# Performance work log

Measured on AMD Instinct MI355X. Metric: run time of the kernel, lower is better.

Reference implementation:

```python
import jax, jax.numpy as jnp
import numpy as np

PATCH = 3
ALPHA = 0.1


def _unfold3x3(x):
    # x: [B, C, H, W] -> [B, C*9, H, W], torch F.unfold with k=3, pad=1, stride=1
    B, C, H, W = x.shape
    p = PATCH // 2
    xp = jnp.pad(x, ((0, 0), (0, 0), (p, p), (p, p)))
    shifts = [xp[:, :, i:i + H, j:j + W] for i in range(PATCH) for j in range(PATCH)]
    # torch unfold orders (C, kh, kw); ordering is irrelevant for the dot-product
    # correlation, but we match it anyway: stack kernel positions after channel.
    out = jnp.stack(shifts, axis=2)  # [B, C, 9, H, W]
    return out.reshape(B, C * PATCH * PATCH, H, W)


def setup_inputs() -> dict:
    key = jax.random.key(0)
    k1, k2 = jax.random.split(key)
    x_lab = jax.random.normal(k1, (4, 3, 64, 64), dtype=jnp.float32)
    feature = jax.random.normal(k2, (4, 64, 64, 64), dtype=jnp.float32)
    return {"x_lab": x_lab, "feature": feature}


def reference(x_lab, feature):
    # scale_factor=1 and feature already at (H, W): both interpolates are identity.
    B, _, H, W = x_lab.shape
    N = H * W
    x_ab = x_lab.reshape(B, 3, N).transpose(0, 2, 1)          # [B, N, 3]
    lf = _unfold3x3(feature).reshape(B, -1, N)                 # [B, C*9, N]
    corr = jnp.einsum('bcn,bcm->bnm', lf, lf)                  # [B, N, N]
    attn = jax.nn.softmax(corr / ALPHA, axis=-1)
    weighted = jnp.einsum('bnm,bmc->bnc', attn, x_ab)          # [B, N, 3]
    return weighted.transpose(0, 2, 1).reshape(B, 3, H, W)
```

## Files before the change

kernel.cpp:

```cpp
#include <hip/hip_runtime.h>


#define NPIX 4096
#define ROWCH 528
#define ROWB  (ROWCH * 16)
#define SCALE 10.0f

typedef __attribute__((ext_vector_type(8))) short bf16x8;
typedef __attribute__((ext_vector_type(4))) float f32x4;

#define MF(a, b, c) __builtin_amdgcn_mfma_f32_16x16x32_bf16(a, b, c, 0, 0, 0)

__device__ __forceinline__ uint4 pack8(const float* v) {
    unsigned h[8];
#pragma unroll
    for (int j = 0; j < 8; ++j) {
        unsigned u = __float_as_uint(v[j]);
        u = u + 0x7fffu + ((u >> 16) & 1u);
        h[j] = u >> 16;
    }
    return (uint4){h[0] | (h[1] << 16), h[2] | (h[3] << 16),
                   h[4] | (h[5] << 16), h[6] | (h[7] << 16)};
}

__device__ __forceinline__ void load_row(const float* fr, int kc, int x, float* L) {
#pragma unroll
    for (int j = 0; j < 8; ++j) L[j] = fr[(size_t)(kc * 8 + j) * NPIX + x];
}

#define MFMA_GRP(T, DBASE) do {                                               \
    _Pragma("unroll")                                                         \
    for (int dx = 0; dx < 3; ++dx)                                            \
        _Pragma("unroll")                                                     \
        for (int ks = 0; ks < 2; ++ks)                                        \
            acc[T] = MF(AF[((DBASE) + dx) * 2 + ks], Bf[ks][dx], acc[T]);     \
} while (0)

#define RETIRE(S, myv) do {                                                   \
    const int kx = kq * 16 + nl;                                              \
    const float xv0 = xls[(myv) * 64 + kx];                                   \
    const float xv1 = xls[NPIX + (myv) * 64 + kx];                            \
    const float xv2 = xls[2 * NPIX + (myv) * 64 + kx];                        \
    _Pragma("unroll")                                                         \
    for (int rg = 0; rg < 4; ++rg) {                                          \
        const float e = __expf(fmaf(acc[S][rg], SCALE, negM[rg]));            \
        l_[rg] += e;                                                          \
        A0[rg] = fmaf(e, xv0, A0[rg]);                                        \
        A1[rg] = fmaf(e, xv1, A1[rg]);                                        \
        A2[rg] = fmaf(e, xv2, A2[rg]);                                        \
    }                                                                         \
    acc[S] = (f32x4){0.f, 0.f, 0.f, 0.f};                                     \
} while (0)

#define STEP(RM, SN, SR, rr) do {                                             \
    const int r_ = (rr);                                                      \
    if (r_ <= 61) *(uint4*)(ring + (SR) * ROWB + wu16) = pack8(L);            \
    if (r_ <= 60) load_row(featb + (r_ + 3) * 64, kc, x, L);                  \
    if (r_ < 64) {                                                            \
        const char* base = ring + (RM) * ROWB + bu;                           \
        bf16x8 Bf[2][3];                                                      \
        _Pragma("unroll")                                                     \
        for (int ks = 0; ks < 2; ++ks) {                                      \
            const char* p = base + ks * 4224;                                 \
            Bf[ks][0] = *(const bf16x8*)(p);                                  \
            Bf[ks][1] = *(const bf16x8*)(p + 16);                             \
            Bf[ks][2] = *(const bf16x8*)(p + 32);                             \
        }                                                                     \
        if (r_ >= 1)     MFMA_GRP(SR, 6);           \
        MFMA_GRP(RM, 3);                                    \
        if (r_ + 1 < 64) MFMA_GRP(SN, 0);                   \
    }                                                                         \
    if (r_ >= 1 && r_ <= 64) RETIRE(SR, r_ - 1);                              \
    if (r_ < 64) __syncthreads();                                             \
} while (0)

__global__ __launch_bounds__(512, 2)
void nlwa_fused(const float* __restrict__ x_lab,
                const float* __restrict__ feature,
                float* __restrict__ out)
{
    __shared__ __align__(16) char ring[3 * ROWB];
    __shared__ float xls[3 * NPIX];
    __shared__ __align__(16) char aux[6144];
    __shared__ float ssq[3][64];
    const int tid = threadIdx.x;
    const int bid = blockIdx.x;
    const int b = bid >> 7, ny = (bid >> 1) & 63, qh = bid & 1;
    const int w = tid >> 6, lane = tid & 63;
    const int quad = lane >> 4, nl = lane & 15;
    const int qg = w & 1, kq = w >> 1;
    const int qofs = qh * 32 + qg * 16;
    const int kc = w, x = lane;
    const int wu16 = (kc * 66 + x + 1) * 16;
    const int bu = (quad * 66 + kq * 16 + nl) * 16;

    const float* featb = feature + (size_t)b * 64 * NPIX;
    const float* xb = x_lab + (size_t)b * 3 * NPIX;
    float* part = (float*)aux;

    {
        const float4* s4 = (const float4*)xb;
        float4* d4 = (float4*)xls;
        for (int i = tid; i < 3 * NPIX / 4; i += 512) d4[i] = s4[i];
    }
    if (tid < 48) {
        const int sl = tid / 16, pu = tid % 16;
        const int u = (pu >> 1) * 66 + (pu & 1) * 65;
        *(uint4*)(ring + sl * ROWB + u * 16) = (uint4){0u, 0u, 0u, 0u};
    }

    float L[8];
#pragma unroll
    for (int dyi = 0; dyi < 3; ++dyi) {
        const int qr = ny + dyi - 1;
        float ss = 0.f;
        if (qr >= 0 && qr < 64) {
            load_row(featb + qr * 64, kc, x, L);
#pragma unroll
            for (int j = 0; j < 8; ++j) ss = fmaf(L[j], L[j], ss);
            *(uint4*)(ring + dyi * ROWB + wu16) = pack8(L);
        } else {
            *(uint4*)(ring + dyi * ROWB + wu16) = (uint4){0u, 0u, 0u, 0u};
        }
        part[(dyi * 8 + kc) * 64 + x] = ss;
    }
    __syncthreads();

    if (tid < 192) {
        const int dyi = tid >> 6, xx = tid & 63;
        float s = 0.f;
#pragma unroll
        for (int k = 0; k < 8; ++k) s += part[(dyi * 8 + k) * 64 + xx];
        ssq[dyi][xx] = s;
    }

    bf16x8 AF[18];
#pragma unroll
    for (int dyi = 0; dyi < 3; ++dyi)
#pragma unroll
        for (int dx = 0; dx < 3; ++dx)
#pragma unroll
            for (int ks = 0; ks < 2; ++ks)
                AF[(dyi * 3 + dx) * 2 + ks] = *(const bf16x8*)(ring + dyi * ROWB +
                    ((quad + ks * 4) * 66 + qofs + nl + dx) * 16);
    __syncthreads();

    float negM[4];
#pragma unroll
    for (int rg = 0; rg < 4; ++rg) {
        const int q = qofs + quad * 4 + rg;
        float a = 0.f;
#pragma unroll
        for (int dyi = 0; dyi < 3; ++dyi)
#pragma unroll
            for (int dx = -1; dx <= 1; ++dx) {
                const int cx = q + dx;
                a += (cx >= 0 && cx < 64) ? ssq[dyi][cx] : 0.f;
            }
        negM[rg] = -SCALE * a;
    }

#pragma unroll
    for (int rr = 0; rr < 2; ++rr) {
        load_row(featb + rr * 64, kc, x, L);
        *(uint4*)(ring + rr * ROWB + wu16) = pack8(L);
    }
    load_row(featb + 2 * 64, kc, x, L);

    float l_[4], A0[4], A1[4], A2[4];
#pragma unroll
    for (int rg = 0; rg < 4; ++rg) { l_[rg] = 0.f; A0[rg] = 0.f; A1[rg] = 0.f; A2[rg] = 0.f; }
    f32x4 acc[3];
#pragma unroll
    for (int i = 0; i < 3; ++i) acc[i] = (f32x4){0.f, 0.f, 0.f, 0.f};
    __syncthreads();

    for (int rb = 0; rb < 66; rb += 3) {
        STEP(0, 1, 2, rb);
        STEP(1, 2, 0, rb + 1);
        STEP(2, 0, 1, rb + 2);
    }

#pragma unroll
    for (int rg = 0; rg < 4; ++rg) {
#pragma unroll
        for (int off = 8; off >= 1; off >>= 1) {
            l_[rg] += __shfl_down(l_[rg], off, 16);
            A0[rg] += __shfl_down(A0[rg], off, 16);
            A1[rg] += __shfl_down(A1[rg], off, 16);
            A2[rg] += __shfl_down(A2[rg], off, 16);
        }
    }
    __syncthreads();
    float4* scrF = (float4*)aux;
    if (nl == 0) {
#pragma unroll
        for (int rg = 0; rg < 4; ++rg) {
            const int ql = qg * 16 + quad * 4 + rg;
            scrF[ql * 4 + kq] = make_float4(l_[rg], A0[rg], A1[rg], A2[rg]);
        }
    }
    __syncthreads();
    if (tid < 32) {
        const float4 t0 = scrF[tid * 4 + 0], t1 = scrF[tid * 4 + 1];
        const float4 t2 = scrF[tid * 4 + 2], t3 = scrF[tid * 4 + 3];
        const float inv = 1.0f / (t0.x + t1.x + t2.x + t3.x);
        float* o = out + (size_t)b * 3 * NPIX + ny * 64 + qh * 32 + tid;
        o[0]        = (t0.y + t1.y + t2.y + t3.y) * inv;
        o[NPIX]     = (t0.z + t1.z + t2.z + t3.z) * inv;
        o[2 * NPIX] = (t0.w + t1.w + t2.w + t3.w) * inv;
    }
}

extern "C" void kernel_launch(void* const* d_in, const int* in_sizes, int n_in,
                              void* d_out, int out_size, void* d_ws, size_t ws_size,
                              hipStream_t stream) {
    (void)in_sizes; (void)n_in; (void)out_size; (void)d_ws; (void)ws_size;
    const float* x_lab   = (const float*)d_in[0];
    const float* feature = (const float*)d_in[1];
    float* out = (float*)d_out;
    nlwa_fused<<<dim3(512), dim3(512), 0, stream>>>(x_lab, feature, out);
}
```

Measured before the change: 155.4 us.

## Merge query halves into one 1024-thread block per image row

```diff
diff --git a/kernel.cpp b/kernel.cpp
--- a/kernel.cpp
+++ b/kernel.cpp
@@ -11,21 +11,20 @@
 
 #define MF(a, b, c) __builtin_amdgcn_mfma_f32_16x16x32_bf16(a, b, c, 0, 0, 0)
 
-__device__ __forceinline__ uint4 pack8(const float* v) {
-    unsigned h[8];
-#pragma unroll
-    for (int j = 0; j < 8; ++j) {
+__device__ __forceinline__ uint2 pack4(const float* v) {
+    unsigned h[4];
+#pragma unroll
+    for (int j = 0; j < 4; ++j) {
         unsigned u = __float_as_uint(v[j]);
         u = u + 0x7fffu + ((u >> 16) & 1u);
         h[j] = u >> 16;
     }
-    return (uint4){h[0] | (h[1] << 16), h[2] | (h[3] << 16),
-                   h[4] | (h[5] << 16), h[6] | (h[7] << 16)};
-}
-
-__device__ __forceinline__ void load_row(const float* fr, int kc, int x, float* L) {
-#pragma unroll
-    for (int j = 0; j < 8; ++j) L[j] = fr[(size_t)(kc * 8 + j) * NPIX + x];
+    return (uint2){h[0] | (h[1] << 16), h[2] | (h[3] << 16)};
+}
+
+__device__ __forceinline__ void load_half(const float* fr, int cb, int x, float* L) {
+#pragma unroll
+    for (int j = 0; j < 4; ++j) L[j] = fr[(size_t)(cb + j) * NPIX + x];
 }
 
 #define MFMA_GRP(T, DBASE) do {                                               \
@@ -54,8 +53,8 @@
 
 #define STEP(RM, SN, SR, rr) do {                                             \
     const int r_ = (rr);                                                      \
-    if (r_ <= 61) *(uint4*)(ring + (SR) * ROWB + wu16) = pack8(L);            \
-    if (r_ <= 60) load_row(featb + (r_ + 3) * 64, kc, x, L);                  \
+    if (r_ <= 61) *(uint2*)(ring + (SR) * ROWB + wu16) = pack4(L);            \
+    if (r_ <= 60) load_half(featb + (r_ + 3) * 64, cb, x, L);                 \
     if (r_ < 64) {                                                            \
         const char* base = ring + (RM) * ROWB + bu;                           \
         bf16x8 Bf[2][3];                                                      \
@@ -74,24 +73,25 @@
     if (r_ < 64) __syncthreads();                                             \
 } while (0)
 
-__global__ __launch_bounds__(512, 2)
+__global__ __launch_bounds__(1024, 1)
 void nlwa_fused(const float* __restrict__ x_lab,
                 const float* __restrict__ feature,
                 float* __restrict__ out)
 {
     __shared__ __align__(16) char ring[3 * ROWB];
     __shared__ float xls[3 * NPIX];
-    __shared__ __align__(16) char aux[6144];
+    __shared__ __align__(16) char aux[12288];
     __shared__ float ssq[3][64];
+
     const int tid = threadIdx.x;
-    const int bid = blockIdx.x;
-    const int b = bid >> 7, ny = (bid >> 1) & 63, qh = bid & 1;
+    const int b = blockIdx.x >> 6, ny = blockIdx.x & 63;
     const int w = tid >> 6, lane = tid & 63;
     const int quad = lane >> 4, nl = lane & 15;
-    const int qg = w & 1, kq = w >> 1;
-    const int qofs = qh * 32 + qg * 16;
-    const int kc = w, x = lane;
-    const int wu16 = (kc * 66 + x + 1) * 16;
+    const int qg = w & 3, kq = w >> 2;
+    const int qofs = qg * 16;
+    const int u = tid >> 1, kc = u >> 6, x = u & 63, half = tid & 1;
+    const int cb = kc * 8 + half * 4;
+    const int wu16 = (kc * 66 + x + 1) * 16 + half * 8;
     const int bu = (quad * 66 + kq * 16 + nl) * 16;
 
     const float* featb = feature + (size_t)b * 64 * NPIX;
@@ -101,28 +101,28 @@
     {
         const float4* s4 = (const float4*)xb;
         float4* d4 = (float4*)xls;
-        for (int i = tid; i < 3 * NPIX / 4; i += 512) d4[i] = s4[i];
+        for (int i = tid; i < 3 * NPIX / 4; i += 1024) d4[i] = s4[i];
     }
     if (tid < 48) {
         const int sl = tid / 16, pu = tid % 16;
-        const int u = (pu >> 1) * 66 + (pu & 1) * 65;
-        *(uint4*)(ring + sl * ROWB + u * 16) = (uint4){0u, 0u, 0u, 0u};
-    }
-
-    float L[8];
+        const int uu = (pu >> 1) * 66 + (pu & 1) * 65;
+        *(uint4*)(ring + sl * ROWB + uu * 16) = (uint4){0u, 0u, 0u, 0u};
+    }
+
+    float L[4];
 #pragma unroll
     for (int dyi = 0; dyi < 3; ++dyi) {
         const int qr = ny + dyi - 1;
         float ss = 0.f;
         if (qr >= 0 && qr < 64) {
-            load_row(featb + qr * 64, kc, x, L);
-#pragma unroll
-            for (int j = 0; j < 8; ++j) ss = fmaf(L[j], L[j], ss);
-            *(uint4*)(ring + dyi * ROWB + wu16) = pack8(L);
+            load_half(featb + qr * 64, cb, x, L);
+#pragma unroll
+            for (int j = 0; j < 4; ++j) ss = fmaf(L[j], L[j], ss);
+            *(uint2*)(ring + dyi * ROWB + wu16) = pack4(L);
         } else {
-            *(uint4*)(ring + dyi * ROWB + wu16) = (uint4){0u, 0u, 0u, 0u};
+            *(uint2*)(ring + dyi * ROWB + wu16) = (uint2){0u, 0u};
         }
-        part[(dyi * 8 + kc) * 64 + x] = ss;
+        part[(dyi * 16 + kc * 2 + half) * 64 + x] = ss;
     }
     __syncthreads();
 
@@ -130,7 +130,7 @@
         const int dyi = tid >> 6, xx = tid & 63;
         float s = 0.f;
 #pragma unroll
-        for (int k = 0; k < 8; ++k) s += part[(dyi * 8 + k) * 64 + xx];
+        for (int k = 0; k < 16; ++k) s += part[(dyi * 16 + k) * 64 + xx];
         ssq[dyi][xx] = s;
     }
 
@@ -162,10 +162,10 @@
 
 #pragma unroll
     for (int rr = 0; rr < 2; ++rr) {
-        load_row(featb + rr * 64, kc, x, L);
-        *(uint4*)(ring + rr * ROWB + wu16) = pack8(L);
-    }
-    load_row(featb + 2 * 64, kc, x, L);
+        load_half(featb + rr * 64, cb, x, L);
+        *(uint2*)(ring + rr * ROWB + wu16) = pack4(L);
+    }
+    load_half(featb + 2 * 64, cb, x, L);
 
     float l_[4], A0[4], A1[4], A2[4];
 #pragma unroll
@@ -196,16 +196,16 @@
     if (nl == 0) {
 #pragma unroll
         for (int rg = 0; rg < 4; ++rg) {
-            const int ql = qg * 16 + quad * 4 + rg;
-            scrF[ql * 4 + kq] = make_float4(l_[rg], A0[rg], A1[rg], A2[rg]);
+            const int q = qofs + quad * 4 + rg;
+            scrF[q * 4 + kq] = make_float4(l_[rg], A0[rg], A1[rg], A2[rg]);
         }
     }
     __syncthreads();
-    if (tid < 32) {
+    if (tid < 64) {
         const float4 t0 = scrF[tid * 4 + 0], t1 = scrF[tid * 4 + 1];
         const float4 t2 = scrF[tid * 4 + 2], t3 = scrF[tid * 4 + 3];
         const float inv = 1.0f / (t0.x + t1.x + t2.x + t3.x);
-        float* o = out + (size_t)b * 3 * NPIX + ny * 64 + qh * 32 + tid;
+        float* o = out + (size_t)b * 3 * NPIX + ny * 64 + tid;
         o[0]        = (t0.y + t1.y + t2.y + t3.y) * inv;
         o[NPIX]     = (t0.z + t1.z + t2.z + t3.z) * inv;
         o[2 * NPIX] = (t0.w + t1.w + t2.w + t3.w) * inv;
@@ -219,5 +219,5 @@
     const float* x_lab   = (const float*)d_in[0];
     const float* feature = (const float*)d_in[1];
     float* out = (float*)d_out;
-    nlwa_fused<<<dim3(512), dim3(512), 0, stream>>>(x_lab, feature, out);
-}
+    nlwa_fused<<<dim3(256), dim3(1024), 0, stream>>>(x_lab, feature, out);
+}
```

Result: slower. 396.6 us (+155.2%).
